# Kernel tuning notes

Hardware: AMD Instinct MI355X
Metric: run time of the kernel (lower is better)

Reference implementation:

```python
import jax, jax.numpy as jnp
import numpy as np

T, B, IN, H, L = 512, 64, 512, 512, 2
GATE = 4 * H


def setup_inputs() -> dict:
    key = jax.random.key(0)
    ks = jax.random.split(key, 8)
    s_in = 1.0 / np.sqrt(IN)
    s_h = 1.0 / np.sqrt(H)
    return {
        "x": jax.random.normal(ks[0], (T, B, IN), dtype=jnp.float32),
        # layer 0 params (nn.Linear stores weight as [out, in]; y = x @ W.T + b)
        "Wi0": jax.random.uniform(ks[1], (GATE, IN), jnp.float32, -s_in, s_in),
        "bi0": jax.random.uniform(ks[2], (GATE,), jnp.float32, -s_in, s_in),
        "Wh0": jax.random.uniform(ks[3], (GATE, H), jnp.float32, -s_h, s_h),
        # layer 1 params
        "Wi1": jax.random.uniform(ks[4], (GATE, H), jnp.float32, -s_h, s_h),
        "bi1": jax.random.uniform(ks[5], (GATE,), jnp.float32, -s_h, s_h),
        "Wh1": jax.random.uniform(ks[6], (GATE, H), jnp.float32, -s_h, s_h),
    }


def _run_layer(x_seq, Wi, bi, Wh):
    """Scan the subLSTM cell over time. x_seq: [T, B, in] -> [T, B, H]."""
    Bs = x_seq.shape[1]
    h0 = jnp.zeros((Bs, H), x_seq.dtype)
    c0 = jnp.zeros((Bs, H), x_seq.dtype)

    def cell(carry, x_t):
        h, c = carry
        # all four gates are sigmoid in subLSTM
        g = jax.nn.sigmoid(x_t @ Wi.T + bi + h @ Wh.T)  # [B, 4H]
        in_gate, out_gate, z_t, f_gate = jnp.split(g, 4, axis=-1)
        c_new = c * f_gate + z_t - in_gate          # subtractive combine
        h_new = jax.nn.sigmoid(c_new) - out_gate    # subtractive output
        return (h_new, c_new), h_new

    (_, _), out = jax.lax.scan(cell, (h0, c0), x_seq)
    return out


def reference(x, Wi0, bi0, Wh0, Wi1, bi1, Wh1):
    out = _run_layer(x, Wi0, bi0, Wh0)
    out = _run_layer(out, Wi1, bi1, Wh1)
    return out  # [T, B, H] (batch_first=False, dropout=0)
```

## Files before the change

### kernel.cpp

```cpp
#include <hip/hip_runtime.h>
#include <stdint.h>

#define TSTEPS 512
#define BATCH  64
#define HDIM   512
#define GATE   2048
#define ACTMAT (BATCH * HDIM)
#define SENT   0xFFFFFFFFu

typedef __attribute__((ext_vector_type(8))) _Float16 f16x8;
typedef __attribute__((ext_vector_type(4))) float f32x4;
typedef __attribute__((ext_vector_type(4))) uint32_t u32x4;

__device__ __forceinline__ unsigned short f2h(float f) {
  union { _Float16 h; unsigned short u; } v;
  v.h = (_Float16)f;
  return v.u;
}
__device__ __forceinline__ float fsigmoid(float x) {
  return 1.0f / (1.0f + __expf(-x));
}


__global__ void init_h(unsigned short* h0, unsigned short* h1) {
  size_t u = (size_t)blockIdx.x * blockDim.x + threadIdx.x;
  u32x4 v;
  if (u < (ACTMAT * 2 / 16)) v = (u32x4){0u, 0u, 0u, 0u};
  else                       v = (u32x4){SENT, SENT, SENT, SENT};
  ((u32x4*)h0)[u] = v;
  ((u32x4*)h1)[u] = v;
}

__global__ void convert_x(const float* __restrict__ x, unsigned short* __restrict__ xh) {
  size_t i = (size_t)(blockIdx.x * blockDim.x + threadIdx.x) * 4;
  float4 v = *(const float4*)(x + i);
  ushort4 o = make_ushort4(f2h(v.x), f2h(v.y), f2h(v.z), f2h(v.w));
  *(ushort4*)(xh + i) = o;
}

__global__ void split_w(const float* __restrict__ Wi, const float* __restrict__ Wh,
                        unsigned short* __restrict__ Wf) {
  int i = blockIdx.x * blockDim.x + threadIdx.x;
  int G = i >> 10, k = i & 1023;
  float w = (k < 512) ? Wi[((size_t)G << 9) + k] : Wh[((size_t)G << 9) + (k - 512)];
  Wf[i] = f2h(w);
}


__global__ __launch_bounds__(256, 1)
void sublstm_persistent(const unsigned short* __restrict__ xh,
                        unsigned short* h0, unsigned short* h1,
                        const unsigned short* __restrict__ Wf0,
                        const unsigned short* __restrict__ Wf1,
                        const float* __restrict__ bi0, const float* __restrict__ bi1,
                        float* __restrict__ out)
{
  __shared__ unsigned short wlds[32][1024];

  const int wg    = blockIdx.x;
  const int layer = wg >> 6;
  const int slice = wg & 63;
  const int j0    = slice << 3;
  const int tid   = threadIdx.x;
  const int lane  = tid & 63;
  const int wv    = tid >> 6;

  const unsigned short* Wf = layer ? Wf1 : Wf0;
  const float* bi = layer ? bi1 : bi0;

  for (int idx = tid; idx < 4096; idx += 256) {
    int n = (idx >> 7) & 31;
    int u = idx & 127;
    int G = ((n & 3) << 9) + j0 + ((((n & 15) >> 2)) << 1) + (n >> 4);
    const unsigned short* s = Wf + ((size_t)G << 10) + ((size_t)u << 3);
    *(uint4*)&wlds[n][(u ^ (n & 15)) << 3] = *(const uint4*)s;
  }
  __syncthreads();

  const int c15 = lane & 15;
  const int g4  = lane >> 4;
  const int n0 = c15, n1 = 16 + c15;
  const int sw = c15;
  const int b    = (wv << 4) + c15;
  const int jcol0 = j0 + (g4 << 1);
  const size_t arow = (size_t)b * HDIM;
  const size_t hoff0 = arow + jcol0;

  const float b00 = bi[jcol0],        b01 = bi[512 + jcol0];
  const float b02 = bi[1024 + jcol0], b03 = bi[1536 + jcol0];
  const float b10 = bi[jcol0 + 1],        b11 = bi[512 + jcol0 + 1];
  const float b12 = bi[1024 + jcol0 + 1], b13 = bi[1536 + jcol0 + 1];

  float c0 = 0.0f, c1 = 0.0f;

#define CONSUME(R, KK, UB) do {                                                        \
    f16x8 a = __builtin_bit_cast(f16x8, (R));                                          \
    int u_ = ((UB) + ((KK) << 2) + g4) ^ sw;                                           \
    f16x8 w0 = *(const f16x8*)&wlds[n0][u_ << 3];                                      \
    f16x8 w1 = *(const f16x8*)&wlds[n1][u_ << 3];                                      \
    acc0 = __builtin_amdgcn_mfma_f32_16x16x32_f16(w0, a, acc0, 0, 0, 0);               \
    acc1 = __builtin_amdgcn_mfma_f32_16x16x32_f16(w1, a, acc1, 0, 0, 0);               \
  } while (0)

#define CONSUME_ALL(P, UB)                                                             \
    CONSUME(P##0, 0, UB);  CONSUME(P##1, 1, UB);  CONSUME(P##2, 2, UB);                \
    CONSUME(P##3, 3, UB);  CONSUME(P##4, 4, UB);  CONSUME(P##5, 5, UB);                \
    CONSUME(P##6, 6, UB);  CONSUME(P##7, 7, UB);  CONSUME(P##8, 8, UB);                \
    CONSUME(P##9, 9, UB);  CONSUME(P##10, 10, UB); CONSUME(P##11, 11, UB);             \
    CONSUME(P##12, 12, UB); CONSUME(P##13, 13, UB); CONSUME(P##14, 14, UB);            \
    CONSUME(P##15, 15, UB)

#define LD1(R, OFFTOK, HP)                                                             \
    asm volatile("global_load_dwordx4 %0, %1, off " OFFTOK " sc0 sc1"                  \
                 : "=v"(R) : "v"(HP) : "memory")

#define ISSUE16(HP, P) do {                                                            \
    LD1(P##0, "", HP);            LD1(P##1, "offset:64", HP);                          \
    LD1(P##2, "offset:128", HP);  LD1(P##3, "offset:192", HP);                         \
    LD1(P##4, "offset:256", HP);  LD1(P##5, "offset:320", HP);                         \
    LD1(P##6, "offset:384", HP);  LD1(P##7, "offset:448", HP);                         \
    LD1(P##8, "offset:512", HP);  LD1(P##9, "offset:576", HP);                         \
    LD1(P##10, "offset:640", HP); LD1(P##11, "offset:704", HP);                        \
    LD1(P##12, "offset:768", HP); LD1(P##13, "offset:832", HP);                        \
    LD1(P##14, "offset:896", HP); LD1(P##15, "offset:960", HP);                        \
  } while (0)

#define BAD1(R) ((R[0] == SENT) | (R[1] == SENT) | (R[2] == SENT) | (R[3] == SENT))

#define VALIDATE(HP, P) do {                                                           \
    for (;;) {                                                                         \
      asm volatile("s_waitcnt vmcnt(0)" ::: "memory");                                 \
      __builtin_amdgcn_sched_barrier(0);                                               \
      int bad_ = BAD1(P##0) | BAD1(P##1) | BAD1(P##2) | BAD1(P##3) |                   \
                 BAD1(P##4) | BAD1(P##5) | BAD1(P##6) | BAD1(P##7) |                   \
                 BAD1(P##8) | BAD1(P##9) | BAD1(P##10) | BAD1(P##11) |                 \
                 BAD1(P##12) | BAD1(P##13) | BAD1(P##14) | BAD1(P##15);                \
      if (!__any(bad_)) break;                                                         \
      ISSUE16(HP, P);                                                                  \
    }                                                                                  \
    __builtin_amdgcn_sched_barrier(0);                                                 \
  } while (0)

#define KHALF_X(AP) do {                                                               \
    const unsigned short* ap_ = (AP) + arow + (g4 << 3);                               \
    _Pragma("unroll")                                                                  \
    for (int kk = 0; kk < 16; ++kk) {                                                  \
      u32x4 rr = *(const u32x4*)(ap_ + (kk << 5));                                     \
      CONSUME(rr, kk, 0);                                                              \
    }                                                                                  \
  } while (0)

#define EPILOGUE(T) do {                                                               \
    unsigned short* hn = (layer ? h1 : h0) + (size_t)((T) + 1) * ACTMAT;               \
    float gi0 = fsigmoid(acc0[0] + b00), go0 = fsigmoid(acc0[1] + b01);                \
    float gz0 = fsigmoid(acc0[2] + b02), gf0 = fsigmoid(acc0[3] + b03);                \
    c0 = c0 * gf0 + gz0 - gi0;                                                         \
    float hv0 = fsigmoid(c0) - go0;                                                    \
    float gi1 = fsigmoid(acc1[0] + b10), go1 = fsigmoid(acc1[1] + b11);                \
    float gz1 = fsigmoid(acc1[2] + b12), gf1 = fsigmoid(acc1[3] + b13);                \
    c1 = c1 * gf1 + gz1 - gi1;                                                         \
    float hv1 = fsigmoid(c1) - go1;                                                    \
    uint32_t hw = (uint32_t)f2h(hv0) | ((uint32_t)f2h(hv1) << 16);                     \
    __hip_atomic_store((uint32_t*)(hn + hoff0), hw, __ATOMIC_RELAXED,                  \
                       __HIP_MEMORY_SCOPE_AGENT);                                      \
    if (layer) {                                                                       \
      float* outp = out + (size_t)(T) * ACTMAT;                                        \
      *(float2*)(outp + hoff0) = make_float2(hv0, hv1);                                \
    }                                                                                  \
  } while (0)

  if (layer == 0) {
    for (int t = 0; t < TSTEPS; ++t) {
      f32x4 acc0 = {}, acc1 = {};
      u32x4 ra0, ra1, ra2, ra3, ra4, ra5, ra6, ra7,
            ra8, ra9, ra10, ra11, ra12, ra13, ra14, ra15;
      const unsigned short* hp = h0 + (size_t)t * ACTMAT + arow + (g4 << 3);
      ISSUE16(hp, ra);
      KHALF_X(xh + (size_t)t * ACTMAT);
      VALIDATE(hp, ra);
      CONSUME_ALL(ra, 64);
      EPILOGUE(t);
    }
  } else {
    for (int t = 0; t < TSTEPS; ++t) {
      f32x4 acc0 = {}, acc1 = {};
      u32x4 ra0, ra1, ra2, ra3, ra4, ra5, ra6, ra7,
            ra8, ra9, ra10, ra11, ra12, ra13, ra14, ra15;
      u32x4 rb0, rb1, rb2, rb3, rb4, rb5, rb6, rb7,
            rb8, rb9, rb10, rb11, rb12, rb13, rb14, rb15;
      const unsigned short* hpA = h1 + (size_t)t * ACTMAT + arow + (g4 << 3);
      const unsigned short* hpB = h0 + (size_t)(t + 1) * ACTMAT + arow + (g4 << 3);
      ISSUE16(hpA, ra);
      ISSUE16(hpB, rb);
      VALIDATE(hpA, ra);
      CONSUME_ALL(ra, 64);
      VALIDATE(hpB, rb);
      CONSUME_ALL(rb, 0);
      EPILOGUE(t);
    }
  }
#undef CONSUME
#undef CONSUME_ALL
#undef LD1
#undef ISSUE16
#undef BAD1
#undef VALIDATE
#undef KHALF_X
#undef EPILOGUE
}


extern "C" void kernel_launch(void* const* d_in, const int* in_sizes, int n_in,
                              void* d_out, int out_size, void* d_ws, size_t ws_size,
                              hipStream_t stream) {
  (void)in_sizes; (void)n_in; (void)out_size; (void)ws_size;
  const float* x   = (const float*)d_in[0];
  const float* Wi0 = (const float*)d_in[1];
  const float* bi0 = (const float*)d_in[2];
  const float* Wh0 = (const float*)d_in[3];
  const float* Wi1 = (const float*)d_in[4];
  const float* bi1 = (const float*)d_in[5];
  const float* Wh1 = (const float*)d_in[6];
  float* out = (float*)d_out;

  char* ws = (char*)d_ws;
  size_t off = 0;
  auto take = [&](size_t bytes) -> void* {
    void* p = ws + off;
    off += (bytes + 255) & ~(size_t)255;
    return p;
  };
  unsigned short* xh  = (unsigned short*)take((size_t)TSTEPS * ACTMAT * 2);
  unsigned short* h0  = (unsigned short*)take((size_t)(TSTEPS + 1) * ACTMAT * 2);
  unsigned short* h1  = (unsigned short*)take((size_t)(TSTEPS + 1) * ACTMAT * 2);
  unsigned short* Wf0 = (unsigned short*)take((size_t)GATE * 1024 * 2);
  unsigned short* Wf1 = (unsigned short*)take((size_t)GATE * 1024 * 2);

  init_h<<<dim3(8208), dim3(256), 0, stream>>>(h0, h1);
  convert_x<<<dim3(16384), dim3(256), 0, stream>>>(x, xh);
  split_w<<<dim3(8192), dim3(256), 0, stream>>>(Wi0, Wh0, Wf0);
  split_w<<<dim3(8192), dim3(256), 0, stream>>>(Wi1, Wh1, Wf1);
  sublstm_persistent<<<dim3(128), dim3(256), 0, stream>>>(
      xh, h0, h1, Wf0, Wf1, bi0, bi1, out);
}
```

Measured before the change: 4.719 ms.

## Retile persistent LSTM workgroups to 16 hidden units by 32 batch rows

Each workgroup now owns 16 hidden columns and half the batch (32 rows) instead of 8 columns and the full batch. It runs 2 waves instead of 4, and each wave issues 4 MFMAs per activation load instead of 2. This doubles weight reuse per activation fetch and halves the activation rows each wave loads per step. The epilogue emits one packed 8-byte h store and one float4 output store per lane instead of narrower stores. The cost is fewer waves per CU for latency hiding, 128 KB of LDS per workgroup, and more accumulator registers. The h store also changes from a relaxed agent-scope atomic to an inline-asm dwordx2 store, which could affect the sentinel-based validation.

```diff
diff --git a/kernel.cpp b/kernel.cpp
--- a/kernel.cpp
+++ b/kernel.cpp
@@ -7,10 +7,12 @@
 #define GATE   2048
 #define ACTMAT (BATCH * HDIM)
 #define SENT   0xFFFFFFFFu
+#define NWORK  128
 
 typedef __attribute__((ext_vector_type(8))) _Float16 f16x8;
 typedef __attribute__((ext_vector_type(4))) float f32x4;
 typedef __attribute__((ext_vector_type(4))) uint32_t u32x4;
+typedef __attribute__((ext_vector_type(2))) uint32_t u32x2;
 
 __device__ __forceinline__ unsigned short f2h(float f) {
   union { _Float16 h; unsigned short u; } v;
@@ -47,7 +49,7 @@
 }
 
 
-__global__ __launch_bounds__(256, 1)
+__global__ __launch_bounds__(128, 1)
 void sublstm_persistent(const unsigned short* __restrict__ xh,
                         unsigned short* h0, unsigned short* h1,
                         const unsigned short* __restrict__ Wf0,
@@ -55,51 +57,57 @@
                         const float* __restrict__ bi0, const float* __restrict__ bi1,
                         float* __restrict__ out)
 {
-  __shared__ unsigned short wlds[32][1024];
+  __shared__ unsigned short wlds[64][1024];
 
   const int wg    = blockIdx.x;
+  const int tid   = threadIdx.x;
   const int layer = wg >> 6;
-  const int slice = wg & 63;
-  const int j0    = slice << 3;
-  const int tid   = threadIdx.x;
+  const int wgl   = wg & 63;
+  const int s     = wgl & 31;
+  const int p     = wgl >> 5;
+  const int j0    = s << 4;
+  const int b0    = p << 5;
   const int lane  = tid & 63;
-  const int wv    = tid >> 6;
+  const int wr    = tid >> 6;
 
   const unsigned short* Wf = layer ? Wf1 : Wf0;
   const float* bi = layer ? bi1 : bi0;
 
-  for (int idx = tid; idx < 4096; idx += 256) {
-    int n = (idx >> 7) & 31;
+  for (int idx = tid; idx < 8192; idx += 128) {
+    int n = idx >> 7;
     int u = idx & 127;
-    int G = ((n & 3) << 9) + j0 + ((((n & 15) >> 2)) << 1) + (n >> 4);
-    const unsigned short* s = Wf + ((size_t)G << 10) + ((size_t)u << 3);
-    *(uint4*)&wlds[n][(u ^ (n & 15)) << 3] = *(const uint4*)s;
+    int G = ((n >> 4) << 9) + j0 + (n & 15);
+    const unsigned short* sp = Wf + ((size_t)G << 10) + ((size_t)u << 3);
+    *(uint4*)&wlds[n][(u ^ (n & 15)) << 3] = *(const uint4*)sp;
   }
   __syncthreads();
 
   const int c15 = lane & 15;
   const int g4  = lane >> 4;
-  const int n0 = c15, n1 = 16 + c15;
-  const int sw = c15;
-  const int b    = (wv << 4) + c15;
-  const int jcol0 = j0 + (g4 << 1);
-  const size_t arow = (size_t)b * HDIM;
-  const size_t hoff0 = arow + jcol0;
-
-  const float b00 = bi[jcol0],        b01 = bi[512 + jcol0];
-  const float b02 = bi[1024 + jcol0], b03 = bi[1536 + jcol0];
-  const float b10 = bi[jcol0 + 1],        b11 = bi[512 + jcol0 + 1];
-  const float b12 = bi[1024 + jcol0 + 1], b13 = bi[1536 + jcol0 + 1];
-
-  float c0 = 0.0f, c1 = 0.0f;
+  const int sw  = c15;
+  const int brow = b0 + (wr << 4) + c15;
+  const int jb   = j0 + (g4 << 2);
+  const size_t arow = (size_t)brow * HDIM;
+  const size_t hoff = arow + jb;
+
+  const float4 bq0 = *(const float4*)&bi[jb];
+  const float4 bq1 = *(const float4*)&bi[512 + jb];
+  const float4 bq2 = *(const float4*)&bi[1024 + jb];
+  const float4 bq3 = *(const float4*)&bi[1536 + jb];
+
+  float cs0 = 0.0f, cs1 = 0.0f, cs2 = 0.0f, cs3 = 0.0f;
 
 #define CONSUME(R, KK, UB) do {                                                        \
     f16x8 a = __builtin_bit_cast(f16x8, (R));                                          \
     int u_ = ((UB) + ((KK) << 2) + g4) ^ sw;                                           \
-    f16x8 w0 = *(const f16x8*)&wlds[n0][u_ << 3];                                      \
-    f16x8 w1 = *(const f16x8*)&wlds[n1][u_ << 3];                                      \
+    f16x8 w0 = *(const f16x8*)&wlds[c15][u_ << 3];                                     \
+    f16x8 w1 = *(const f16x8*)&wlds[16 + c15][u_ << 3];                                \
+    f16x8 w2 = *(const f16x8*)&wlds[32 + c15][u_ << 3];                                \
+    f16x8 w3 = *(const f16x8*)&wlds[48 + c15][u_ << 3];                                \
     acc0 = __builtin_amdgcn_mfma_f32_16x16x32_f16(w0, a, acc0, 0, 0, 0);               \
     acc1 = __builtin_amdgcn_mfma_f32_16x16x32_f16(w1, a, acc1, 0, 0, 0);               \
+    acc2 = __builtin_amdgcn_mfma_f32_16x16x32_f16(w2, a, acc2, 0, 0, 0);               \
+    acc3 = __builtin_amdgcn_mfma_f32_16x16x32_f16(w3, a, acc3, 0, 0, 0);               \
   } while (0)
 
 #define CONSUME_ALL(P, UB)                                                             \
@@ -152,26 +160,33 @@
 
 #define EPILOGUE(T) do {                                                               \
     unsigned short* hn = (layer ? h1 : h0) + (size_t)((T) + 1) * ACTMAT;               \
-    float gi0 = fsigmoid(acc0[0] + b00), go0 = fsigmoid(acc0[1] + b01);                \
-    float gz0 = fsigmoid(acc0[2] + b02), gf0 = fsigmoid(acc0[3] + b03);                \
-    c0 = c0 * gf0 + gz0 - gi0;                                                         \
-    float hv0 = fsigmoid(c0) - go0;                                                    \
-    float gi1 = fsigmoid(acc1[0] + b10), go1 = fsigmoid(acc1[1] + b11);                \
-    float gz1 = fsigmoid(acc1[2] + b12), gf1 = fsigmoid(acc1[3] + b13);                \
-    c1 = c1 * gf1 + gz1 - gi1;                                                         \
-    float hv1 = fsigmoid(c1) - go1;                                                    \
-    uint32_t hw = (uint32_t)f2h(hv0) | ((uint32_t)f2h(hv1) << 16);                     \
-    __hip_atomic_store((uint32_t*)(hn + hoff0), hw, __ATOMIC_RELAXED,                  \
-                       __HIP_MEMORY_SCOPE_AGENT);                                      \
+    float gi_, go_, gz_, gf_, h0v, h1v, h2v, h3v;                                      \
+    gi_ = fsigmoid(acc0[0] + bq0.x); go_ = fsigmoid(acc1[0] + bq1.x);                  \
+    gz_ = fsigmoid(acc2[0] + bq2.x); gf_ = fsigmoid(acc3[0] + bq3.x);                  \
+    cs0 = cs0 * gf_ + gz_ - gi_;  h0v = fsigmoid(cs0) - go_;                           \
+    gi_ = fsigmoid(acc0[1] + bq0.y); go_ = fsigmoid(acc1[1] + bq1.y);                  \
+    gz_ = fsigmoid(acc2[1] + bq2.y); gf_ = fsigmoid(acc3[1] + bq3.y);                  \
+    cs1 = cs1 * gf_ + gz_ - gi_;  h1v = fsigmoid(cs1) - go_;                           \
+    gi_ = fsigmoid(acc0[2] + bq0.z); go_ = fsigmoid(acc1[2] + bq1.z);                  \
+    gz_ = fsigmoid(acc2[2] + bq2.z); gf_ = fsigmoid(acc3[2] + bq3.z);                  \
+    cs2 = cs2 * gf_ + gz_ - gi_;  h2v = fsigmoid(cs2) - go_;                           \
+    gi_ = fsigmoid(acc0[3] + bq0.w); go_ = fsigmoid(acc1[3] + bq1.w);                  \
+    gz_ = fsigmoid(acc2[3] + bq2.w); gf_ = fsigmoid(acc3[3] + bq3.w);                  \
+    cs3 = cs3 * gf_ + gz_ - gi_;  h3v = fsigmoid(cs3) - go_;                           \
+    u32x2 dv;                                                                          \
+    dv[0] = (uint32_t)f2h(h0v) | ((uint32_t)f2h(h1v) << 16);                           \
+    dv[1] = (uint32_t)f2h(h2v) | ((uint32_t)f2h(h3v) << 16);                           \
+    asm volatile("global_store_dwordx2 %0, %1, off sc0 sc1"                            \
+                 :: "v"((uint32_t*)(hn + hoff)), "v"(dv) : "memory");                  \
     if (layer) {                                                                       \
       float* outp = out + (size_t)(T) * ACTMAT;                                        \
-      *(float2*)(outp + hoff0) = make_float2(hv0, hv1);                                \
+      *(float4*)(outp + hoff) = make_float4(h0v, h1v, h2v, h3v);                       \
     }                                                                                  \
   } while (0)
 
   if (layer == 0) {
     for (int t = 0; t < TSTEPS; ++t) {
-      f32x4 acc0 = {}, acc1 = {};
+      f32x4 acc0 = {}, acc1 = {}, acc2 = {}, acc3 = {};
       u32x4 ra0, ra1, ra2, ra3, ra4, ra5, ra6, ra7,
             ra8, ra9, ra10, ra11, ra12, ra13, ra14, ra15;
       const unsigned short* hp = h0 + (size_t)t * ACTMAT + arow + (g4 << 3);
@@ -183,7 +198,7 @@
     }
   } else {
     for (int t = 0; t < TSTEPS; ++t) {
-      f32x4 acc0 = {}, acc1 = {};
+      f32x4 acc0 = {}, acc1 = {}, acc2 = {}, acc3 = {};
       u32x4 ra0, ra1, ra2, ra3, ra4, ra5, ra6, ra7,
             ra8, ra9, ra10, ra11, ra12, ra13, ra14, ra15;
       u32x4 rb0, rb1, rb2, rb3, rb4, rb5, rb6, rb7,
@@ -240,6 +255,6 @@
   convert_x<<<dim3(16384), dim3(256), 0, stream>>>(x, xh);
   split_w<<<dim3(8192), dim3(256), 0, stream>>>(Wi0, Wh0, Wf0);
   split_w<<<dim3(8192), dim3(256), 0, stream>>>(Wi1, Wh1, Wf1);
-  sublstm_persistent<<<dim3(128), dim3(256), 0, stream>>>(
+  sublstm_persistent<<<dim3(NWORK), dim3(128), 0, stream>>>(
       xh, h0, h1, Wf0, Wf1, bi0, bi1, out);
 }
```

After: 3.869 ms. 1.22x faster.
